# Kernel optimization log

Hardware: AMD Instinct MI355X
Metric: run time of the kernel (lower is better)

The kernel has to match this reference:

```python
import jax, jax.numpy as jnp
import numpy as np

QMIN, QMAX = -128.0, 127.0


def setup_inputs() -> dict:
    key = jax.random.key(0)
    k1, k2, k3, k4, k5 = jax.random.split(key, 5)
    B, S, IN, OUT = 4, 2048, 4096, 11008
    hidden_states = jax.random.normal(k1, (B, S, IN), dtype=jnp.float16)
    # symmetric per-channel int8 weights (stored as int32 for harness compat)
    weight = jax.random.randint(k2, (OUT, IN), -128, 128, dtype=jnp.int32)
    weight_scale = jax.random.uniform(k3, (OUT,), dtype=jnp.float32, minval=0.001, maxval=0.02)
    input_scale = jax.random.uniform(k4, (1,), dtype=jnp.float32, minval=0.01, maxval=0.05)
    pre_quant_scale = jax.random.uniform(k5, (IN,), dtype=jnp.float32, minval=0.5, maxval=1.5).astype(jnp.float16)
    return {
        "hidden_states": hidden_states,
        "weight": weight,
        "weight_scale": weight_scale,
        "input_scale": input_scale,
        "pre_quant_scale": pre_quant_scale,
    }


def reference(hidden_states, weight, weight_scale, input_scale, pre_quant_scale):
    # SmoothQuant smoothing (fp16 elementwise Mul)
    x_smooth = hidden_states * pre_quant_scale  # [B,S,IN] fp16
    # Per-tensor activation fake-quant (Q + DQ), done in fp32 like QuantizeLinear
    s = input_scale.astype(jnp.float32)  # [1]
    q = jnp.clip(jnp.round(x_smooth.astype(jnp.float32) / s), QMIN, QMAX)
    x_dq = (q * s).astype(jnp.float16)  # [B,S,IN]
    # Per-channel weight dequant (axis=0 -> out_features)
    w_dq = (weight.astype(jnp.float32) * weight_scale[:, None]).astype(jnp.float16)  # [OUT,IN]
    # F.linear: x @ W^T  (emulated int8 GEMM in fp16)
    return jnp.einsum('bsi,oi->bso', x_dq, w_dq)
```

## Files before the change

kernel.cpp:

```cpp
#include <hip/hip_runtime.h>
#include <hip/hip_fp16.h>
#include <stdint.h>

typedef int i32x4 __attribute__((ext_vector_type(4)));

#define IN_F  4096
#define OUT_F 11008
#define MROWS 8192
#define BM 256
#define BN 256
#define BKB 64
#define NKT (IN_F / BKB)
#define GRID_M (MROWS / BM)
#define GRID_N (OUT_F / BN)
#define NBLK (GRID_M * GRID_N)
#define QBLKS 16384
#define PBLKS 22016

#define AS1 __attribute__((address_space(1)))
#define AS3 __attribute__((address_space(3)))

__global__ __launch_bounds__(256) void prep_kernel(
    const float* __restrict__ x, const float* __restrict__ pqs,
    const float* __restrict__ iscale, int8_t* __restrict__ q,
    const int* __restrict__ w, int8_t* __restrict__ wq)
{
    const int blk = blockIdx.x;
    if (blk < QBLKS) {
        const int i = blk * 256 + threadIdx.x;
        const float s = iscale[0];
        const size_t base = (size_t)i * 8;
        const int col = (int)(base & (IN_F - 1));

        const float4 x0 = *(const float4*)(x + base);
        const float4 x1 = *(const float4*)(x + base + 4);
        const float4 p0 = *(const float4*)(pqs + col);
        const float4 p1 = *(const float4*)(pqs + col + 4);

        float xs[8];
        xs[0] = x0.x * p0.x; xs[1] = x0.y * p0.y; xs[2] = x0.z * p0.z; xs[3] = x0.w * p0.w;
        xs[4] = x1.x * p1.x; xs[5] = x1.y * p1.y; xs[6] = x1.z * p1.z; xs[7] = x1.w * p1.w;

        unsigned int lo = 0, hi = 0;
        #pragma unroll
        for (int j = 0; j < 8; ++j) {
            float xm = __half2float(__float2half(xs[j]));
            float qf = nearbyintf(xm / s);
            qf = fminf(fmaxf(qf, -128.0f), 127.0f);
            unsigned int b = (unsigned int)((int)qf & 0xff);
            if (j < 4) lo |= b << (8 * j);
            else       hi |= b << (8 * (j - 4));
        }
        *(uint2*)(q + base) = make_uint2(lo, hi);
    } else {
        const size_t i = ((size_t)(blk - QBLKS) * 256 + threadIdx.x) * 8;
        const int4 a = *(const int4*)(w + i);
        const int4 b = *(const int4*)(w + i + 4);
        unsigned int lo = (a.x & 0xff) | ((a.y & 0xff) << 8) | ((a.z & 0xff) << 16) | ((unsigned int)(a.w & 0xff) << 24);
        unsigned int hi = (b.x & 0xff) | ((b.y & 0xff) << 8) | ((b.z & 0xff) << 16) | ((unsigned int)(b.w & 0xff) << 24);
        *(uint2*)(wq + i) = make_uint2(lo, hi);
    }
}

__global__ __launch_bounds__(1024, 4) void gemm_i8_256_kernel(
    const int8_t* __restrict__ Aq,
    const int8_t* __restrict__ Wq,
    const float* __restrict__ wscale,
    const float* __restrict__ iscale,
    float* __restrict__ out)
{
    __shared__ int8_t lds[131072];

    const int tid  = threadIdx.x;
    const int lane = tid & 63;
    const int wv   = tid >> 6;
    const int wr   = wv >> 2;
    const int wc   = wv & 3;

    const int bid = (int)blockIdx.x;
    const int swz = (bid & 7) * (NBLK / 8) + (bid >> 3);
    const int bm = swz / GRID_N;
    const int bn = swz % GRID_N;
    const int brow = bm * BM, bcol = bn * BN;

    const int8_t* Ab = Aq + (size_t)brow * IN_F;
    const int8_t* Bb = Wq + (size_t)bcol * IN_F;

    const int srow = tid >> 2;
    const int scol = ((tid & 3) ^ ((srow >> 1) & 3)) * 16;
    const int sdst = tid * 16;

    #define STAGE_A(t) __builtin_amdgcn_global_load_lds( \
        (const AS1 void*)(Ab + (size_t)srow * IN_F + (t) * BKB + scol), \
        (AS3 void*)(lds + ((t) & 3) * 32768 + sdst), 16, 0, 0)
    #define STAGE_B(t) __builtin_amdgcn_global_load_lds( \
        (const AS1 void*)(Bb + (size_t)srow * IN_F + (t) * BKB + scol), \
        (AS3 void*)(lds + ((t) & 3) * 32768 + 16384 + sdst), 16, 0, 0)

    i32x4 acc[4][4] = {};
    i32x4 a[4], b[4];

    const int rl = lane & 15;
    const int hk = lane >> 4;
    const int koff = (hk ^ ((rl >> 1) & 3)) * 16;
    const int a_base = (wr * 64 + rl) * 64;
    const int b_base = (wc * 64 + rl) * 64;

    STAGE_A(0); STAGE_B(0);
    STAGE_A(1); STAGE_B(1);
    STAGE_A(2); STAGE_B(2);
    asm volatile("s_waitcnt vmcnt(4)" ::: "memory");
    __builtin_amdgcn_s_barrier();
    #pragma unroll
    for (int mf = 0; mf < 4; ++mf)
        a[mf] = *(const i32x4*)(lds + a_base + mf * 1024 + koff);
    #pragma unroll
    for (int nf = 0; nf < 4; ++nf)
        b[nf] = *(const i32x4*)(lds + 16384 + b_base + nf * 1024 + koff);

    for (int kt = 0; kt < NKT; ++kt) {
        if (kt + 2 < NKT) asm volatile("s_waitcnt vmcnt(2)" ::: "memory");
        else              asm volatile("s_waitcnt vmcnt(0)" ::: "memory");
        asm volatile("s_waitcnt lgkmcnt(0)" ::: "memory");
        __builtin_amdgcn_s_barrier();

        if (kt + 3 < NKT) { STAGE_A(kt + 3); STAGE_B(kt + 3); }

        __builtin_amdgcn_sched_barrier(0);

        const int8_t* An = lds + ((kt + 1) & 3) * 32768;
        const int8_t* Bn = An + 16384;
        const bool more = (kt + 1 < NKT);

        #pragma unroll
        for (int mf = 0; mf < 4; ++mf) {
            #pragma unroll
            for (int nf = 0; nf < 4; ++nf)
                acc[mf][nf] = __builtin_amdgcn_mfma_i32_16x16x64_i8(a[mf], b[nf], acc[mf][nf], 0, 0, 0);
            if (more)
                a[mf] = *(const i32x4*)(An + a_base + mf * 1024 + koff);
        }
        if (more) {
            #pragma unroll
            for (int nf = 0; nf < 4; ++nf)
                b[nf] = *(const i32x4*)(Bn + b_base + nf * 1024 + koff);
        }
        __builtin_amdgcn_sched_barrier(0);
    }

    const float s = iscale[0];
    #pragma unroll
    for (int nf = 0; nf < 4; ++nf) {
        const int col = bcol + wc * 64 + nf * 16 + rl;
        const float sc = s * wscale[col];
        #pragma unroll
        for (int mf = 0; mf < 4; ++mf) {
            const int r0 = brow + wr * 64 + mf * 16 + hk * 4;
            #pragma unroll
            for (int j = 0; j < 4; ++j)
                out[(size_t)(r0 + j) * OUT_F + col] = (float)acc[mf][nf][j] * sc;
        }
    }
    #undef STAGE_A
    #undef STAGE_B
}

__global__ __launch_bounds__(256) void simple_ref_kernel(
    const float* __restrict__ x, const int* __restrict__ w,
    const float* __restrict__ wsc, const float* __restrict__ isc,
    const float* __restrict__ pqs, float* __restrict__ out)
{
    const float s = isc[0];
    const int m = blockIdx.x;
    const int o = blockIdx.y * 256 + threadIdx.x;
    if (o >= OUT_F) return;
    const float wso = wsc[o];
    const float* xr = x + (size_t)m * IN_F;
    const int* wr = w + (size_t)o * IN_F;
    float acc = 0.0f;
    for (int k = 0; k < IN_F; ++k) {
        float xm = __half2float(__float2half(xr[k] * pqs[k]));
        float qf = nearbyintf(xm / s);
        qf = fminf(fmaxf(qf, -128.0f), 127.0f);
        float xdq = __half2float(__float2half(qf * s));
        float wdq = __half2float(__float2half((float)wr[k] * wso));
        acc = fmaf(xdq, wdq, acc);
    }
    out[(size_t)m * OUT_F + o] = acc;
}

extern "C" void kernel_launch(void* const* d_in, const int* in_sizes, int n_in,
                              void* d_out, int out_size, void* d_ws, size_t ws_size,
                              hipStream_t stream)
{
    const float* x   = nullptr;
    const int*   w   = nullptr;
    const float* wsc = nullptr;
    const float* isc = nullptr;
    const float* pqs = nullptr;
    for (int i = 0; i < n_in; ++i) {
        switch (in_sizes[i]) {
            case MROWS * IN_F:   x   = (const float*)d_in[i]; break;
            case OUT_F * IN_F:   w   = (const int*)d_in[i];   break;
            case OUT_F:          wsc = (const float*)d_in[i]; break;
            case 1:              isc = (const float*)d_in[i]; break;
            case IN_F:           pqs = (const float*)d_in[i]; break;
        }
    }
    float* out = (float*)d_out;

    const size_t need = (size_t)MROWS * IN_F + (size_t)OUT_F * IN_F;
    if (d_ws == nullptr || ws_size < need) {
        dim3 grid(MROWS, (OUT_F + 255) / 256);
        simple_ref_kernel<<<grid, 256, 0, stream>>>(x, w, wsc, isc, pqs, out);
        return;
    }

    int8_t* Aq = (int8_t*)d_ws;
    int8_t* Wq = Aq + (size_t)MROWS * IN_F;

    prep_kernel<<<QBLKS + PBLKS, 256, 0, stream>>>(x, pqs, isc, Aq, w, Wq);
    gemm_i8_256_kernel<<<NBLK, 1024, 0, stream>>>(Aq, Wq, wsc, isc, out);
}
```

Baseline: 470.2 us.

## Shrink GEMM tile to 128x256 with 512 threads and triple-buffered LDS

Reduces the block tile from 256x256 (1024 threads, 4 LDS stages of 32KB) to 128x256 (512 threads, 3 stages of 24KB), loading B with two async loads per thread. The software register prefetch of the next k-tile's fragments and the sched_barriers are removed; fragments are now loaded from LDS right before the MFMAs in each iteration. The smaller LDS footprint is meant to let more blocks reside per CU and raise occupancy. In exchange it adds global traffic per FLOP because each tile now has less reuse, and it drops the LDS/MFMA overlap that the prefetch provided.

```diff
diff --git a/kernel.cpp b/kernel.cpp
--- a/kernel.cpp
+++ b/kernel.cpp
@@ -7,7 +7,7 @@
 #define IN_F  4096
 #define OUT_F 11008
 #define MROWS 8192
-#define BM 256
+#define BM 128
 #define BN 256
 #define BKB 64
 #define NKT (IN_F / BKB)
@@ -16,6 +16,7 @@
 #define NBLK (GRID_M * GRID_N)
 #define QBLKS 16384
 #define PBLKS 22016
+#define BUFB 24576
 
 #define AS1 __attribute__((address_space(1)))
 #define AS3 __attribute__((address_space(3)))
@@ -62,14 +63,14 @@
     }
 }
 
-__global__ __launch_bounds__(1024, 4) void gemm_i8_256_kernel(
+__global__ __launch_bounds__(512, 4) void gemm_i8_kernel(
     const int8_t* __restrict__ Aq,
     const int8_t* __restrict__ Wq,
     const float* __restrict__ wscale,
     const float* __restrict__ iscale,
     float* __restrict__ out)
 {
-    __shared__ int8_t lds[131072];
+    __shared__ int8_t lds[3 * BUFB];
 
     const int tid  = threadIdx.x;
     const int lane = tid & 63;
@@ -86,19 +87,27 @@
     const int8_t* Ab = Aq + (size_t)brow * IN_F;
     const int8_t* Bb = Wq + (size_t)bcol * IN_F;
 
-    const int srow = tid >> 2;
-    const int scol = ((tid & 3) ^ ((srow >> 1) & 3)) * 16;
-    const int sdst = tid * 16;
-
-    #define STAGE_A(t) __builtin_amdgcn_global_load_lds( \
-        (const AS1 void*)(Ab + (size_t)srow * IN_F + (t) * BKB + scol), \
-        (AS3 void*)(lds + ((t) & 3) * 32768 + sdst), 16, 0, 0)
-    #define STAGE_B(t) __builtin_amdgcn_global_load_lds( \
-        (const AS1 void*)(Bb + (size_t)srow * IN_F + (t) * BKB + scol), \
-        (AS3 void*)(lds + ((t) & 3) * 32768 + 16384 + sdst), 16, 0, 0)
+    const int arow = tid >> 2;
+    const int acol = ((tid & 3) ^ ((arow >> 1) & 3)) * 16;
+    const int adst = tid * 16;
+    int brow_s[2], bcol_s[2], bdst[2];
+    #pragma unroll
+    for (int i = 0; i < 2; ++i) {
+        const int n = i * 512 + tid;
+        brow_s[i] = n >> 2;
+        bcol_s[i] = ((n & 3) ^ ((brow_s[i] >> 1) & 3)) * 16;
+        bdst[i] = n * 16;
+    }
+
+    #define STAGE(t) do { int8_t* Bf = lds + ((t) % 3) * BUFB; \
+        const int k0_ = (t) * BKB; \
+        __builtin_amdgcn_global_load_lds((const AS1 void*)(Ab + (size_t)arow * IN_F + k0_ + acol), \
+                                         (AS3 void*)(Bf + adst), 16, 0, 0); \
+        _Pragma("unroll") for (int i_ = 0; i_ < 2; ++i_) \
+            __builtin_amdgcn_global_load_lds((const AS1 void*)(Bb + (size_t)brow_s[i_] * IN_F + k0_ + bcol_s[i_]), \
+                                             (AS3 void*)(Bf + 8192 + bdst[i_]), 16, 0, 0); } while (0)
 
     i32x4 acc[4][4] = {};
-    i32x4 a[4], b[4];
 
     const int rl = lane & 15;
     const int hk = lane >> 4;
@@ -106,46 +115,31 @@
     const int a_base = (wr * 64 + rl) * 64;
     const int b_base = (wc * 64 + rl) * 64;
 
-    STAGE_A(0); STAGE_B(0);
-    STAGE_A(1); STAGE_B(1);
-    STAGE_A(2); STAGE_B(2);
-    asm volatile("s_waitcnt vmcnt(4)" ::: "memory");
-    __builtin_amdgcn_s_barrier();
-    #pragma unroll
-    for (int mf = 0; mf < 4; ++mf)
-        a[mf] = *(const i32x4*)(lds + a_base + mf * 1024 + koff);
-    #pragma unroll
-    for (int nf = 0; nf < 4; ++nf)
-        b[nf] = *(const i32x4*)(lds + 16384 + b_base + nf * 1024 + koff);
+    STAGE(0);
+    STAGE(1);
 
     for (int kt = 0; kt < NKT; ++kt) {
-        if (kt + 2 < NKT) asm volatile("s_waitcnt vmcnt(2)" ::: "memory");
+        if (kt + 1 < NKT) asm volatile("s_waitcnt vmcnt(3)" ::: "memory");
         else              asm volatile("s_waitcnt vmcnt(0)" ::: "memory");
-        asm volatile("s_waitcnt lgkmcnt(0)" ::: "memory");
         __builtin_amdgcn_s_barrier();
 
-        if (kt + 3 < NKT) { STAGE_A(kt + 3); STAGE_B(kt + 3); }
-
-        __builtin_amdgcn_sched_barrier(0);
-
-        const int8_t* An = lds + ((kt + 1) & 3) * 32768;
-        const int8_t* Bn = An + 16384;
-        const bool more = (kt + 1 < NKT);
-
-        #pragma unroll
-        for (int mf = 0; mf < 4; ++mf) {
+        if (kt + 2 < NKT) STAGE(kt + 2);
+
+        const int8_t* At = lds + (kt % 3) * BUFB;
+        const int8_t* Bt = At + 8192;
+
+        i32x4 a[4], b[4];
+        #pragma unroll
+        for (int mf = 0; mf < 4; ++mf)
+            a[mf] = *(const i32x4*)(At + a_base + mf * 1024 + koff);
+        #pragma unroll
+        for (int nf = 0; nf < 4; ++nf)
+            b[nf] = *(const i32x4*)(Bt + b_base + nf * 1024 + koff);
+        #pragma unroll
+        for (int mf = 0; mf < 4; ++mf)
             #pragma unroll
             for (int nf = 0; nf < 4; ++nf)
                 acc[mf][nf] = __builtin_amdgcn_mfma_i32_16x16x64_i8(a[mf], b[nf], acc[mf][nf], 0, 0, 0);
-            if (more)
-                a[mf] = *(const i32x4*)(An + a_base + mf * 1024 + koff);
-        }
-        if (more) {
-            #pragma unroll
-            for (int nf = 0; nf < 4; ++nf)
-                b[nf] = *(const i32x4*)(Bn + b_base + nf * 1024 + koff);
-        }
-        __builtin_amdgcn_sched_barrier(0);
     }
 
     const float s = iscale[0];
@@ -161,8 +155,7 @@
                 out[(size_t)(r0 + j) * OUT_F + col] = (float)acc[mf][nf][j] * sc;
         }
     }
-    #undef STAGE_A
-    #undef STAGE_B
+    #undef STAGE
 }
 
 __global__ __launch_bounds__(256) void simple_ref_kernel(
@@ -220,5 +213,5 @@
     int8_t* Wq = Aq + (size_t)MROWS * IN_F;
 
     prep_kernel<<<QBLKS + PBLKS, 256, 0, stream>>>(x, pqs, isc, Aq, w, Wq);
-    gemm_i8_256_kernel<<<NBLK, 1024, 0, stream>>>(Aq, Wq, wsc, isc, out);
-}
+    gemm_i8_kernel<<<NBLK, 512, 0, stream>>>(Aq, Wq, wsc, isc, out);
+}
```

Measured after the change: 571.6 us. +21.5%, slower.
